# Kernel optimization log

Hardware: AMD Instinct MI355X
Metric: run time of the kernel (lower is better)

Reference implementation:

```python
import jax, jax.numpy as jnp
import numpy as np

K = 1024          # codebook size
D = 64            # embedding dim
CC = 0.25         # commitment cost


def setup_inputs() -> dict:
    key = jax.random.key(0)
    k1, k2 = jax.random.split(key)
    inputs = jax.random.normal(k1, (64, 64, 32, 32), dtype=jnp.float32)  # [B, C=D, H, W]
    # nn.Embedding weight init: uniform(-1/K, 1/K)
    embedding = jax.random.uniform(k2, (K, D), dtype=jnp.float32,
                                   minval=-1.0 / K, maxval=1.0 / K)
    return {"inputs": inputs, "embedding": embedding}


def reference(inputs, embedding):
    # NCHW -> NHWC
    x = jnp.transpose(inputs, (0, 2, 3, 1))            # [B, H, W, D]
    B, H, W, Dd = x.shape
    flat = x.reshape(-1, Dd)                           # [N, D]
    distances = (jnp.sum(flat * flat, axis=1, keepdims=True)
                 - 2.0 * flat @ embedding.T
                 + jnp.sum(embedding * embedding, axis=1)[None, :])
    encoding_indices = jnp.argmin(distances, axis=1)   # [N]
    encodings = encoding_indices.reshape(B, H, W)      # [B, H, W]
    quantized = embedding[encodings]                   # [B, H, W, D]

    e_latent_loss = jnp.mean((jax.lax.stop_gradient(quantized) - x) ** 2)
    q_latent_loss = jnp.mean((quantized - jax.lax.stop_gradient(x)) ** 2)
    loss = q_latent_loss + CC * e_latent_loss

    # straight-through estimator
    quantized_st = x + jax.lax.stop_gradient(quantized - x)
    out = jnp.transpose(quantized_st, (0, 3, 1, 2))    # NHWC -> NCHW
    nll = jnp.ones((1,), dtype=jnp.float32)
    return out, encodings, loss, nll
```

## Files before the change

kernel.cpp:

```cpp
#include <hip/hip_runtime.h>
#include <stdint.h>

constexpr int KCODES = 1024;
constexpr int DDIM   = 64;
constexpr int HW     = 1024;
constexpr int NPTS   = 65536;
constexpr int PPB    = 64;
constexpr int NBLK   = NPTS / PPB;

constexpr int OUT_IDX  = 4194304;
constexpr int OUT_LOSS = 4259840;
constexpr int OUT_NLL  = 4259841;

constexpr int WS_MAXC  = 0;
constexpr int WS_C     = 16;
constexpr int WS_E     = 2048;
constexpr int WS_PART  = 34816;

typedef __attribute__((ext_vector_type(8))) short short8v;
typedef __attribute__((ext_vector_type(4))) float float4v;

__device__ __forceinline__ uint16_t f2bf(float f) {
    uint32_t u = __float_as_uint(f);
    return (uint16_t)((u + 0x7fffu + ((u >> 16) & 1u)) >> 16);
}
__device__ __forceinline__ uint32_t pack2bf(float a, float b) {
    return (uint32_t)f2bf(a) | ((uint32_t)f2bf(b) << 16);
}

__device__ __forceinline__ float np_pairwise_sumsq64(const float* a) {
    float r[8];
    #pragma unroll
    for (int j = 0; j < 8; ++j) r[j] = __fmul_rn(a[j], a[j]);
    #pragma unroll
    for (int i = 8; i < 64; i += 8)
        #pragma unroll
        for (int j = 0; j < 8; ++j)
            r[j] = __fadd_rn(r[j], __fmul_rn(a[i + j], a[i + j]));
    return __fadd_rn(__fadd_rn(__fadd_rn(r[0], r[1]), __fadd_rn(r[2], r[3])),
                     __fadd_rn(__fadd_rn(r[4], r[5]), __fadd_rn(r[6], r[7])));
}

__global__ __launch_bounds__(64) void vq_init(const float* __restrict__ emb,
                                              float* __restrict__ ws) {
    const int k = blockIdx.x * 64 + threadIdx.x;
    float row[DDIM];
    const float4* src = (const float4*)(emb + (size_t)k * DDIM);
    #pragma unroll
    for (int j = 0; j < 16; ++j) ((float4*)row)[j] = src[j];
    float C = np_pairwise_sumsq64(row);
    ws[WS_C + k] = C;
    {
        const int c = k >> 4, col = k & 15;
        uint32_t* eb = (uint32_t*)ws + WS_E + c * 512;
        #pragma unroll
        for (int q = 0; q < 4; ++q) {
            uint32_t* d0 = eb + (q * 16 + col) * 4;
            uint32_t* d1 = eb + 256 + (q * 16 + col) * 4;
            #pragma unroll
            for (int j = 0; j < 4; ++j) {
                d0[j] = pack2bf(row[q * 8 + 2 * j],      row[q * 8 + 2 * j + 1]);
                d1[j] = pack2bf(row[32 + q * 8 + 2 * j], row[32 + q * 8 + 2 * j + 1]);
            }
        }
    }
    float m = C;
    #pragma unroll
    for (int off = 32; off > 0; off >>= 1) m = fmaxf(m, __shfl_down(m, off, 64));
    if (threadIdx.x == 0) ws[WS_MAXC + blockIdx.x] = m;
}

__global__ __launch_bounds__(256, 4) void vq_main(
        const float* __restrict__ inp, const float* __restrict__ emb,
        float* __restrict__ ws, float* __restrict__ out)
{
    __shared__ float    sAp[PPB][4];
    __shared__ float    sA[PPB];
    __shared__ float    sPart[4][PPB];
    __shared__ float    sThr[PPB];
    __shared__ unsigned long long sCandL[16][PPB];
    __shared__ int      sCntL[16][PPB];
    __shared__ int      sWin[PPB];
    __shared__ float    sred[4];

    const int tid  = threadIdx.x;
    const int lane = tid & 63;
    const int wave = tid >> 6;
    const int col  = lane & 15;
    const int quad = lane >> 4;
    const int base = blockIdx.x * PPB;
    const int b    = base >> 10;
    const int hw0  = base & 1023;

    {
        const int pp = tid >> 2;
        const int jj = (tid & 3) * 2;
        const float* xin = inp + (size_t)b * DDIM * HW + (hw0 + pp);
        float r0, r1;
        {
            float v0 = xin[(size_t)jj * HW];
            float v1 = xin[(size_t)(jj + 1) * HW];
            r0 = __fmul_rn(v0, v0);
            r1 = __fmul_rn(v1, v1);
        }
        #pragma unroll
        for (int i = 8; i < 64; i += 8) {
            float v0 = xin[(size_t)(i + jj) * HW];
            float v1 = xin[(size_t)(i + jj + 1) * HW];
            r0 = __fadd_rn(r0, __fmul_rn(v0, v0));
            r1 = __fadd_rn(r1, __fmul_rn(v1, v1));
        }
        sAp[pp][tid & 3] = __fadd_rn(r0, r1);
    }

    short8v a[4][2];
    #pragma unroll
    for (int g = 0; g < 4; ++g) {
        const float* xp = inp + (size_t)b * DDIM * HW + (hw0 + g * 16 + col);
        short8v t0, t1;
        #pragma unroll
        for (int j = 0; j < 8; ++j) {
            t0[j] = (short)f2bf(xp[(size_t)(quad * 8 + j) * HW]);
            t1[j] = (short)f2bf(xp[(size_t)(32 + quad * 8 + j) * HW]);
        }
        a[g][0] = t0; a[g][1] = t1;
    }

    const char* Eb = (const char*)((const uint32_t*)ws + WS_E);
    const char* Ew = Eb + (size_t)wave * 16 * 2048 + (size_t)lane * 16;
    const float* Cw = ws + WS_C;
    const int k0 = wave * 256;
    const float4v* Cq = (const float4v*)(ws + WS_C + k0);

    float gmax[4] = {-3.0e38f, -3.0e38f, -3.0e38f, -3.0e38f};
    {
        short8v pa0 = *(const short8v*)(Ew);
        short8v pa1 = *(const short8v*)(Ew + 1024);
        short8v pb0 = *(const short8v*)(Ew + 2048);
        short8v pb1 = *(const short8v*)(Ew + 3072);
        float4v ca4 = Cq[quad];
        float4v cb4 = Cq[4 + quad];
        #pragma unroll 1
        for (int c2 = 0; c2 < 16; c2 += 2) {
            short8v u0 = pa0, u1 = pa1; float4v uc4 = ca4;
            if (c2 + 2 < 16) {
                const char* er = Ew + (size_t)(c2 + 2) * 2048;
                pa0 = *(const short8v*)(er);
                pa1 = *(const short8v*)(er + 1024);
                ca4 = Cq[(c2 + 2) * 4 + quad];
            }
            {
                float4v ci = {uc4[0] * -0.5f, uc4[1] * -0.5f,
                              uc4[2] * -0.5f, uc4[3] * -0.5f};
                #pragma unroll
                for (int g = 0; g < 4; ++g) {
                    float4v acc = ci;
                    acc = __builtin_amdgcn_mfma_f32_16x16x32_bf16(u0, a[g][0], acc, 0, 0, 0);
                    acc = __builtin_amdgcn_mfma_f32_16x16x32_bf16(u1, a[g][1], acc, 0, 0, 0);
                    gmax[g] = fmaxf(gmax[g],
                                    fmaxf(fmaxf(acc[0], acc[1]), fmaxf(acc[2], acc[3])));
                }
            }
            short8v v0 = pb0, v1 = pb1; float4v vc4 = cb4;
            if (c2 + 3 < 16) {
                const char* er = Ew + (size_t)(c2 + 3) * 2048;
                pb0 = *(const short8v*)(er);
                pb1 = *(const short8v*)(er + 1024);
                cb4 = Cq[(c2 + 3) * 4 + quad];
            }
            {
                float4v ci = {vc4[0] * -0.5f, vc4[1] * -0.5f,
                              vc4[2] * -0.5f, vc4[3] * -0.5f};
                #pragma unroll
                for (int g = 0; g < 4; ++g) {
                    float4v acc = ci;
                    acc = __builtin_amdgcn_mfma_f32_16x16x32_bf16(v0, a[g][0], acc, 0, 0, 0);
                    acc = __builtin_amdgcn_mfma_f32_16x16x32_bf16(v1, a[g][1], acc, 0, 0, 0);
                    gmax[g] = fmaxf(gmax[g],
                                    fmaxf(fmaxf(acc[0], acc[1]), fmaxf(acc[2], acc[3])));
                }
            }
        }
    }
    #pragma unroll
    for (int g = 0; g < 4; ++g) {
        float m = gmax[g];
        m = fmaxf(m, __shfl_xor(m, 16, 64));
        m = fmaxf(m, __shfl_xor(m, 32, 64));
        if (quad == 0) sPart[wave][g * 16 + col] = m;
    }
    __syncthreads();

    if (tid < PPB) {
        float A = __fadd_rn(__fadd_rn(sAp[tid][0], sAp[tid][1]),
                            __fadd_rn(sAp[tid][2], sAp[tid][3]));
        sA[tid] = A;
        float gm = fmaxf(fmaxf(sPart[0][tid], sPart[1][tid]),
                         fmaxf(sPart[2][tid], sPart[3][tid]));
        float mc = ws[WS_MAXC];
        #pragma unroll
        for (int j = 1; j < 16; ++j) mc = fmaxf(mc, ws[WS_MAXC + j]);
        sThr[tid] = gm - (0.015625f * sqrtf(A) * sqrtf(mc) + 6e-5f);
    }
    __syncthreads();

    float thrg[4];
    #pragma unroll
    for (int g = 0; g < 4; ++g) thrg[g] = sThr[g * 16 + col];

    unsigned long long lst[4] = {0ull, 0ull, 0ull, 0ull};
    int cnt[4] = {0, 0, 0, 0};
    {
        short8v pa0 = *(const short8v*)(Ew);
        short8v pa1 = *(const short8v*)(Ew + 1024);
        short8v pb0 = *(const short8v*)(Ew + 2048);
        short8v pb1 = *(const short8v*)(Ew + 3072);
        float4v ca4 = Cq[quad];
        float4v cb4 = Cq[4 + quad];
        #pragma unroll 1
        for (int c2 = 0; c2 < 16; c2 += 2) {
            short8v u0 = pa0, u1 = pa1; float4v uc4 = ca4;
            if (c2 + 2 < 16) {
                const char* er = Ew + (size_t)(c2 + 2) * 2048;
                pa0 = *(const short8v*)(er);
                pa1 = *(const short8v*)(er + 1024);
                ca4 = Cq[(c2 + 2) * 4 + quad];
            }
            {
                float4v ci = {uc4[0] * -0.5f, uc4[1] * -0.5f,
                              uc4[2] * -0.5f, uc4[3] * -0.5f};
                const int kb = k0 + c2 * 16 + quad * 4;
                #pragma unroll
                for (int g = 0; g < 4; ++g) {
                    float4v acc = ci;
                    acc = __builtin_amdgcn_mfma_f32_16x16x32_bf16(u0, a[g][0], acc, 0, 0, 0);
                    acc = __builtin_amdgcn_mfma_f32_16x16x32_bf16(u1, a[g][1], acc, 0, 0, 0);
                    float m4 = fmaxf(fmaxf(acc[0], acc[1]), fmaxf(acc[2], acc[3]));
                    if (__any(m4 >= thrg[g])) {
                        #pragma unroll
                        for (int r = 0; r < 4; ++r) {
                            if (acc[r] >= thrg[g]) {
                                if (cnt[g] < 4)
                                    lst[g] |= (unsigned long long)(unsigned)(kb + r)
                                              << (cnt[g] << 4);
                                ++cnt[g];
                            }
                        }
                    }
                }
            }
            short8v v0 = pb0, v1 = pb1; float4v vc4 = cb4;
            if (c2 + 3 < 16) {
                const char* er = Ew + (size_t)(c2 + 3) * 2048;
                pb0 = *(const short8v*)(er);
                pb1 = *(const short8v*)(er + 1024);
                cb4 = Cq[(c2 + 3) * 4 + quad];
            }
            {
                float4v ci = {vc4[0] * -0.5f, vc4[1] * -0.5f,
                              vc4[2] * -0.5f, vc4[3] * -0.5f};
                const int kb = k0 + (c2 + 1) * 16 + quad * 4;
                #pragma unroll
                for (int g = 0; g < 4; ++g) {
                    float4v acc = ci;
                    acc = __builtin_amdgcn_mfma_f32_16x16x32_bf16(v0, a[g][0], acc, 0, 0, 0);
                    acc = __builtin_amdgcn_mfma_f32_16x16x32_bf16(v1, a[g][1], acc, 0, 0, 0);
                    float m4 = fmaxf(fmaxf(acc[0], acc[1]), fmaxf(acc[2], acc[3]));
                    if (__any(m4 >= thrg[g])) {
                        #pragma unroll
                        for (int r = 0; r < 4; ++r) {
                            if (acc[r] >= thrg[g]) {
                                if (cnt[g] < 4)
                                    lst[g] |= (unsigned long long)(unsigned)(kb + r)
                                              << (cnt[g] << 4);
                                ++cnt[g];
                            }
                        }
                    }
                }
            }
        }
    }
    {
        const int wq = wave * 4 + quad;
        #pragma unroll
        for (int g = 0; g < 4; ++g) {
            sCandL[wq][g * 16 + col] = lst[g];
            sCntL[wq][g * 16 + col]  = cnt[g];
        }
    }
    __syncthreads();

    if (tid < PPB) {
        const int p = tid, n = base + p;
        int tot = 0, cmax = 0;
        #pragma unroll
        for (int wq = 0; wq < 16; ++wq) {
            int c = sCntL[wq][p];
            tot += c;
            cmax = c > cmax ? c : cmax;
        }
        int win;
        if (tot == 1) {
            win = 0;
            #pragma unroll
            for (int wq = 0; wq < 16; ++wq)
                if (sCntL[wq][p]) win = (int)(sCandL[wq][p] & 0xffffu);
        } else {
            const float* xin = inp + (size_t)b * DDIM * HW + (hw0 + p);
            float x[DDIM];
            #pragma unroll
            for (int d = 0; d < DDIM; ++d) x[d] = xin[(size_t)d * HW];
            const float A = sA[p];
            float bd = 3.0e38f; win = KCODES - 1;
            if (cmax <= 4) {
                #pragma unroll 1
                for (int wq = 0; wq < 16; ++wq) {
                    int c = sCntL[wq][p];
                    unsigned long long L = sCandL[wq][p];
                    #pragma unroll 1
                    for (int i = 0; i < c; ++i) {
                        int k = (int)(L & 0xffffu);
                        L >>= 16;
                        float e[DDIM];
                        const float4* e4 = (const float4*)(emb + (size_t)k * DDIM);
                        #pragma unroll
                        for (int j = 0; j < 16; ++j) ((float4*)e)[j] = e4[j];
                        float g = 0.f;
                        #pragma unroll
                        for (int d = 0; d < DDIM; ++d) g = fmaf(x[d], e[d], g);
                        float dd = __fadd_rn(__fsub_rn(A, __fmul_rn(2.0f, g)), Cw[k]);
                        if (dd < bd || (dd == bd && k < win)) { bd = dd; win = k; }
                    }
                }
            } else {
                #pragma unroll 1
                for (int k = 0; k < KCODES; ++k) {
                    float e[DDIM];
                    const float4* e4 = (const float4*)(emb + (size_t)k * DDIM);
                    #pragma unroll
                    for (int j = 0; j < 16; ++j) ((float4*)e)[j] = e4[j];
                    float g = 0.f;
                    #pragma unroll
                    for (int d = 0; d < DDIM; ++d) g = fmaf(x[d], e[d], g);
                    float dd = __fadd_rn(__fsub_rn(A, __fmul_rn(2.0f, g)), Cw[k]);
                    if (dd < bd) { bd = dd; win = k; }
                }
            }
        }
        sWin[p] = win;
        out[OUT_IDX + n] = (float)win;
    }
    __syncthreads();

    {
        const int pl = tid & 63, qtr = tid >> 6;
        const int win = sWin[pl];
        const int ch0 = qtr * 16;
        float q[16];
        const float4* q4 = (const float4*)(emb + (size_t)win * DDIM + ch0);
        #pragma unroll
        for (int j = 0; j < 4; ++j) ((float4*)q)[j] = q4[j];
        const size_t off = (size_t)b * DDIM * HW + (size_t)ch0 * HW + (hw0 + pl);
        const float* xin2 = inp + off;
        float* orow = out + off;
        float lacc = 0.f;
        #pragma unroll
        for (int j = 0; j < 16; ++j) {
            float xv = xin2[(size_t)j * HW];
            float diff = __fsub_rn(q[j], xv);
            orow[(size_t)j * HW] = __fadd_rn(xv, diff);
            lacc = fmaf(diff, diff, lacc);
        }
        #pragma unroll
        for (int o2 = 32; o2 > 0; o2 >>= 1) lacc += __shfl_down(lacc, o2, 64);
        if (lane == 0) sred[wave] = lacc;
    }
    __syncthreads();
    if (tid == 0)
        ws[WS_PART + blockIdx.x] = sred[0] + sred[1] + sred[2] + sred[3];
}

__global__ __launch_bounds__(256) void vq_fin(const float* __restrict__ ws,
                                              float* __restrict__ out) {
    __shared__ float sred[4];
    const int tid = threadIdx.x;
    float s = 0.f;
    #pragma unroll
    for (int j = 0; j < 4; ++j) s += ws[WS_PART + j * 256 + tid];
    #pragma unroll
    for (int off = 32; off > 0; off >>= 1) s += __shfl_down(s, off, 64);
    if ((tid & 63) == 0) sred[tid >> 6] = s;
    __syncthreads();
    if (tid == 0) {
        float L = sred[0] + sred[1] + sred[2] + sred[3];
        out[OUT_LOSS] = L * (1.25f / 4194304.0f);
        out[OUT_NLL]  = 1.0f;
    }
}

extern "C" void kernel_launch(void* const* d_in, const int* in_sizes, int n_in,
                              void* d_out, int out_size, void* d_ws, size_t ws_size,
                              hipStream_t stream) {
    const float* inp = (const float*)d_in[0];
    const float* emb = (const float*)d_in[1];
    float* out = (float*)d_out;
    float* ws  = (float*)d_ws;

    vq_init<<<16, 64, 0, stream>>>(emb, ws);
    vq_main<<<NBLK, 256, 0, stream>>>(inp, emb, ws, out);
    vq_fin<<<1, 256, 0, stream>>>(ws, out);
}
```

Measured before the change: 114.5 us.

## Fuse max and candidate passes into single MFMA sweep with running-max top-4 slots

```diff
diff --git a/kernel.cpp b/kernel.cpp
--- a/kernel.cpp
+++ b/kernel.cpp
@@ -26,6 +26,36 @@
 }
 __device__ __forceinline__ uint32_t pack2bf(float a, float b) {
     return (uint32_t)f2bf(a) | ((uint32_t)f2bf(b) << 16);
+}
+
+__device__ __forceinline__ uint32_t bf_key(uint16_t b) {
+    return (uint32_t)b ^ (0x8000u + ((uint32_t)(b >> 15) * 0x7FFFu));
+}
+__device__ __forceinline__ float key_to_f32(uint32_t k16) {
+    uint32_t bb = (k16 & 0x8000u) ? (k16 ^ 0x8000u) : (~k16 & 0xFFFFu);
+    return __uint_as_float(bb << 16);
+}
+
+__device__ __forceinline__ void slot_insert(uint32_t& s0, uint32_t& s1,
+                                            uint32_t& s2, uint32_t& s3,
+                                            uint32_t& ovfg, float s, int idx,
+                                            float mnew, float marE) {
+    uint32_t key  = bf_key(f2bf(s));
+    uint32_t slot = (key << 16) | (uint32_t)idx;
+    uint32_t m01 = s0 < s1 ? s0 : s1;
+    uint32_t m23 = s2 < s3 ? s2 : s3;
+    uint32_t mm  = m01 < m23 ? m01 : m23;
+    float mf = key_to_f32(mm >> 16);
+    bool safe = (mm < 0x10000u) || (mf < mnew - marE);
+    ovfg |= safe ? 0u : 1u;
+    bool p0 = (s0 == mm);
+    bool p1 = !p0 && (s1 == mm);
+    bool p2 = !p0 && !p1 && (s2 == mm);
+    bool p3 = !(p0 || p1 || p2);
+    s0 = p0 ? slot : s0;
+    s1 = p1 ? slot : s1;
+    s2 = p2 ? slot : s2;
+    s3 = p3 ? slot : s3;
 }
 
 __device__ __forceinline__ float np_pairwise_sumsq64(const float* a) {
@@ -76,10 +106,13 @@
 {
     __shared__ float    sAp[PPB][4];
     __shared__ float    sA[PPB];
+    __shared__ float    sMar[PPB];
+    __shared__ float    sMarE[PPB];
+    __shared__ float    sEps[PPB];
     __shared__ float    sPart[4][PPB];
     __shared__ float    sThr[PPB];
-    __shared__ unsigned long long sCandL[16][PPB];
-    __shared__ int      sCntL[16][PPB];
+    __shared__ uint32_t sSlot[16][PPB][4];
+    __shared__ uint8_t  sOvf[16][PPB];
     __shared__ int      sWin[PPB];
     __shared__ float    sred[4];
 
@@ -125,6 +158,30 @@
         }
         a[g][0] = t0; a[g][1] = t1;
     }
+    __syncthreads();
+
+    if (tid < PPB) {
+        float A = __fadd_rn(__fadd_rn(sAp[tid][0], sAp[tid][1]),
+                            __fadd_rn(sAp[tid][2], sAp[tid][3]));
+        sA[tid] = A;
+        float mc = ws[WS_MAXC];
+        #pragma unroll
+        for (int j = 1; j < 16; ++j) mc = fmaxf(mc, ws[WS_MAXC + j]);
+        float sq = sqrtf(A) * sqrtf(mc);
+        float M  = 0.015625f * sq + 6e-5f;
+        float E  = 0.0078125f * sq + 0.001953125f * mc;
+        sMar[tid]  = M;
+        sMarE[tid] = M + E;
+        sEps[tid]  = E;
+    }
+    __syncthreads();
+
+    float marg[4], marE[4];
+    #pragma unroll
+    for (int g = 0; g < 4; ++g) {
+        marg[g] = sMar[g * 16 + col];
+        marE[g] = sMarE[g * 16 + col];
+    }
 
     const char* Eb = (const char*)((const uint32_t*)ws + WS_E);
     const char* Ew = Eb + (size_t)wave * 16 * 2048 + (size_t)lane * 16;
@@ -132,7 +189,9 @@
     const int k0 = wave * 256;
     const float4v* Cq = (const float4v*)(ws + WS_C + k0);
 
-    float gmax[4] = {-3.0e38f, -3.0e38f, -3.0e38f, -3.0e38f};
+    float    m_run[4] = {-3.0e38f, -3.0e38f, -3.0e38f, -3.0e38f};
+    uint32_t sl[4][4] = {{0,0,0,0},{0,0,0,0},{0,0,0,0},{0,0,0,0}};
+    uint32_t ovf[4]   = {0,0,0,0};
     {
         short8v pa0 = *(const short8v*)(Ew);
         short8v pa1 = *(const short8v*)(Ew + 1024);
@@ -152,83 +211,6 @@
             {
                 float4v ci = {uc4[0] * -0.5f, uc4[1] * -0.5f,
                               uc4[2] * -0.5f, uc4[3] * -0.5f};
-                #pragma unroll
-                for (int g = 0; g < 4; ++g) {
-                    float4v acc = ci;
-                    acc = __builtin_amdgcn_mfma_f32_16x16x32_bf16(u0, a[g][0], acc, 0, 0, 0);
-                    acc = __builtin_amdgcn_mfma_f32_16x16x32_bf16(u1, a[g][1], acc, 0, 0, 0);
-                    gmax[g] = fmaxf(gmax[g],
-                                    fmaxf(fmaxf(acc[0], acc[1]), fmaxf(acc[2], acc[3])));
-                }
-            }
-            short8v v0 = pb0, v1 = pb1; float4v vc4 = cb4;
-            if (c2 + 3 < 16) {
-                const char* er = Ew + (size_t)(c2 + 3) * 2048;
-                pb0 = *(const short8v*)(er);
-                pb1 = *(const short8v*)(er + 1024);
-                cb4 = Cq[(c2 + 3) * 4 + quad];
-            }
-            {
-                float4v ci = {vc4[0] * -0.5f, vc4[1] * -0.5f,
-                              vc4[2] * -0.5f, vc4[3] * -0.5f};
-                #pragma unroll
-                for (int g = 0; g < 4; ++g) {
-                    float4v acc = ci;
-                    acc = __builtin_amdgcn_mfma_f32_16x16x32_bf16(v0, a[g][0], acc, 0, 0, 0);
-                    acc = __builtin_amdgcn_mfma_f32_16x16x32_bf16(v1, a[g][1], acc, 0, 0, 0);
-                    gmax[g] = fmaxf(gmax[g],
-                                    fmaxf(fmaxf(acc[0], acc[1]), fmaxf(acc[2], acc[3])));
-                }
-            }
-        }
-    }
-    #pragma unroll
-    for (int g = 0; g < 4; ++g) {
-        float m = gmax[g];
-        m = fmaxf(m, __shfl_xor(m, 16, 64));
-        m = fmaxf(m, __shfl_xor(m, 32, 64));
-        if (quad == 0) sPart[wave][g * 16 + col] = m;
-    }
-    __syncthreads();
-
-    if (tid < PPB) {
-        float A = __fadd_rn(__fadd_rn(sAp[tid][0], sAp[tid][1]),
-                            __fadd_rn(sAp[tid][2], sAp[tid][3]));
-        sA[tid] = A;
-        float gm = fmaxf(fmaxf(sPart[0][tid], sPart[1][tid]),
-                         fmaxf(sPart[2][tid], sPart[3][tid]));
-        float mc = ws[WS_MAXC];
-        #pragma unroll
-        for (int j = 1; j < 16; ++j) mc = fmaxf(mc, ws[WS_MAXC + j]);
-        sThr[tid] = gm - (0.015625f * sqrtf(A) * sqrtf(mc) + 6e-5f);
-    }
-    __syncthreads();
-
-    float thrg[4];
-    #pragma unroll
-    for (int g = 0; g < 4; ++g) thrg[g] = sThr[g * 16 + col];
-
-    unsigned long long lst[4] = {0ull, 0ull, 0ull, 0ull};
-    int cnt[4] = {0, 0, 0, 0};
-    {
-        short8v pa0 = *(const short8v*)(Ew);
-        short8v pa1 = *(const short8v*)(Ew + 1024);
-        short8v pb0 = *(const short8v*)(Ew + 2048);
-        short8v pb1 = *(const short8v*)(Ew + 3072);
-        float4v ca4 = Cq[quad];
-        float4v cb4 = Cq[4 + quad];
-        #pragma unroll 1
-        for (int c2 = 0; c2 < 16; c2 += 2) {
-            short8v u0 = pa0, u1 = pa1; float4v uc4 = ca4;
-            if (c2 + 2 < 16) {
-                const char* er = Ew + (size_t)(c2 + 2) * 2048;
-                pa0 = *(const short8v*)(er);
-                pa1 = *(const short8v*)(er + 1024);
-                ca4 = Cq[(c2 + 2) * 4 + quad];
-            }
-            {
-                float4v ci = {uc4[0] * -0.5f, uc4[1] * -0.5f,
-                              uc4[2] * -0.5f, uc4[3] * -0.5f};
                 const int kb = k0 + c2 * 16 + quad * 4;
                 #pragma unroll
                 for (int g = 0; g < 4; ++g) {
@@ -236,16 +218,14 @@
                     acc = __builtin_amdgcn_mfma_f32_16x16x32_bf16(u0, a[g][0], acc, 0, 0, 0);
                     acc = __builtin_amdgcn_mfma_f32_16x16x32_bf16(u1, a[g][1], acc, 0, 0, 0);
                     float m4 = fmaxf(fmaxf(acc[0], acc[1]), fmaxf(acc[2], acc[3]));
-                    if (__any(m4 >= thrg[g])) {
+                    float mnew = fmaxf(m_run[g], m4);
+                    m_run[g] = mnew;
+                    if (__any(m4 >= mnew - marg[g])) {
                         #pragma unroll
-                        for (int r = 0; r < 4; ++r) {
-                            if (acc[r] >= thrg[g]) {
-                                if (cnt[g] < 4)
-                                    lst[g] |= (unsigned long long)(unsigned)(kb + r)
-                                              << (cnt[g] << 4);
-                                ++cnt[g];
-                            }
-                        }
+                        for (int r = 0; r < 4; ++r)
+                            if (acc[r] >= mnew - marg[g])
+                                slot_insert(sl[g][0], sl[g][1], sl[g][2], sl[g][3],
+                                            ovf[g], acc[r], kb + r, mnew, marE[g]);
                     }
                 }
             }
@@ -266,46 +246,90 @@
                     acc = __builtin_amdgcn_mfma_f32_16x16x32_bf16(v0, a[g][0], acc, 0, 0, 0);
                     acc = __builtin_amdgcn_mfma_f32_16x16x32_bf16(v1, a[g][1], acc, 0, 0, 0);
                     float m4 = fmaxf(fmaxf(acc[0], acc[1]), fmaxf(acc[2], acc[3]));
-                    if (__any(m4 >= thrg[g])) {
+                    float mnew = fmaxf(m_run[g], m4);
+                    m_run[g] = mnew;
+                    if (__any(m4 >= mnew - marg[g])) {
                         #pragma unroll
-                        for (int r = 0; r < 4; ++r) {
-                            if (acc[r] >= thrg[g]) {
-                                if (cnt[g] < 4)
-                                    lst[g] |= (unsigned long long)(unsigned)(kb + r)
-                                              << (cnt[g] << 4);
-                                ++cnt[g];
-                            }
-                        }
+                        for (int r = 0; r < 4; ++r)
+                            if (acc[r] >= mnew - marg[g])
+                                slot_insert(sl[g][0], sl[g][1], sl[g][2], sl[g][3],
+                                            ovf[g], acc[r], kb + r, mnew, marE[g]);
                     }
                 }
             }
         }
     }
+    #pragma unroll
+    for (int g = 0; g < 4; ++g) {
+        float m = m_run[g];
+        m = fmaxf(m, __shfl_xor(m, 16, 64));
+        m = fmaxf(m, __shfl_xor(m, 32, 64));
+        if (quad == 0) sPart[wave][g * 16 + col] = m;
+    }
     {
         const int wq = wave * 4 + quad;
         #pragma unroll
         for (int g = 0; g < 4; ++g) {
-            sCandL[wq][g * 16 + col] = lst[g];
-            sCntL[wq][g * 16 + col]  = cnt[g];
-        }
+            uint32_t* d = &sSlot[wq][g * 16 + col][0];
+            d[0] = sl[g][0]; d[1] = sl[g][1]; d[2] = sl[g][2]; d[3] = sl[g][3];
+            sOvf[wq][g * 16 + col] = (uint8_t)ovf[g];
+        }
+    }
+    __syncthreads();
+
+    if (tid < PPB) {
+        float gm = fmaxf(fmaxf(sPart[0][tid], sPart[1][tid]),
+                         fmaxf(sPart[2][tid], sPart[3][tid]));
+        sThr[tid] = gm - sMar[tid];
     }
     __syncthreads();
 
     if (tid < PPB) {
         const int p = tid, n = base + p;
-        int tot = 0, cmax = 0;
-        #pragma unroll
+        const float thrE = sThr[p] - sEps[p];
+        bool ovfAny = false;
+        #pragma unroll
+        for (int wq = 0; wq < 16; ++wq) ovfAny |= (sOvf[wq][p] != 0);
+        int tot = 0, first = 0;
+        #pragma unroll 1
         for (int wq = 0; wq < 16; ++wq) {
-            int c = sCntL[wq][p];
-            tot += c;
-            cmax = c > cmax ? c : cmax;
+            #pragma unroll
+            for (int j = 0; j < 4; ++j) {
+                uint32_t s = sSlot[wq][p][j];
+                float f = key_to_f32(s >> 16);
+                if (f >= thrE) { ++tot; if (tot == 1) first = (int)(s & 0xFFFFu); }
+            }
         }
         int win;
-        if (tot == 1) {
-            win = 0;
+        if (!ovfAny && tot == 1) {
+            win = first;
+        } else if (!ovfAny && tot >= 2) {
+            const float* xin = inp + (size_t)b * DDIM * HW + (hw0 + p);
+            float x[DDIM];
             #pragma unroll
-            for (int wq = 0; wq < 16; ++wq)
-                if (sCntL[wq][p]) win = (int)(sCandL[wq][p] & 0xffffu);
+            for (int d = 0; d < DDIM; ++d) x[d] = xin[(size_t)d * HW];
+            const float A = sA[p];
+            float bd = 3.0e38f; win = KCODES - 1;
+            #pragma unroll 1
+            for (int wq = 0; wq < 16; ++wq) {
+                #pragma unroll
+                for (int j = 0; j < 4; ++j) {
+                    uint32_t s = sSlot[wq][p][j];
+                    float f = key_to_f32(s >> 16);
+                    if (f >= thrE) {
+                        int k = (int)(s & 0xFFFFu);
+                        float e[DDIM];
+                        const float4* e4 = (const float4*)(emb + (size_t)k * DDIM);
+                        #pragma unroll
+                        for (int jj = 0; jj < 16; ++jj) ((float4*)e)[jj] = e4[jj];
+                        float g = 0.f;
+                        #pragma unroll
+                        for (int d = 0; d < DDIM; ++d) g = fmaf(x[d], e[d], g);
+                        float dd = __fadd_rn(__fsub_rn(A, __fmul_rn(2.0f, g)), Cw[k]);
+                        if (dd < bd || (dd == bd && k < win)) { bd = dd; win = k; }
+                    }
+                }
+            }
         } else {
             const float* xin = inp + (size_t)b * DDIM * HW + (hw0 + p);
             float x[DDIM];
@@ -313,39 +337,17 @@
             for (int d = 0; d < DDIM; ++d) x[d] = xin[(size_t)d * HW];
             const float A = sA[p];
             float bd = 3.0e38f; win = KCODES - 1;
-            if (cmax <= 4) {
-                #pragma unroll 1
-                for (int wq = 0; wq < 16; ++wq) {
-                    int c = sCntL[wq][p];
-                    unsigned long long L = sCandL[wq][p];
-                    #pragma unroll 1
-                    for (int i = 0; i < c; ++i) {
-                        int k = (int)(L & 0xffffu);
-                        L >>= 16;
-                        float e[DDIM];
-                        const float4* e4 = (const float4*)(emb + (size_t)k * DDIM);
-                        #pragma unroll
-                        for (int j = 0; j < 16; ++j) ((float4*)e)[j] = e4[j];
-                        float g = 0.f;
-                        #pragma unroll
-                        for (int d = 0; d < DDIM; ++d) g = fmaf(x[d], e[d], g);
-                        float dd = __fadd_rn(__fsub_rn(A, __fmul_rn(2.0f, g)), Cw[k]);
-                        if (dd < bd || (dd == bd && k < win)) { bd = dd; win = k; }
-                    }
-                }
-            } else {
-                #pragma unroll 1
-                for (int k = 0; k < KCODES; ++k) {
-                    float e[DDIM];
-                    const float4* e4 = (const float4*)(emb + (size_t)k * DDIM);
-                    #pragma unroll
-                    for (int j = 0; j < 16; ++j) ((float4*)e)[j] = e4[j];
-                    float g = 0.f;
-                    #pragma unroll
-                    for (int d = 0; d < DDIM; ++d) g = fmaf(x[d], e[d], g);
-                    float dd = __fadd_rn(__fsub_rn(A, __fmul_rn(2.0f, g)), Cw[k]);
-                    if (dd < bd) { bd = dd; win = k; }
-                }
+            #pragma unroll 1
+            for (int k = 0; k < KCODES; ++k) {
+                float e[DDIM];
+                const float4* e4 = (const float4*)(emb + (size_t)k * DDIM);
+                #pragma unroll
+                for (int j = 0; j < 16; ++j) ((float4*)e)[j] = e4[j];
+                float g = 0.f;
+                #pragma unroll
+                for (int d = 0; d < DDIM; ++d) g = fmaf(x[d], e[d], g);
+                float dd = __fadd_rn(__fsub_rn(A, __fmul_rn(2.0f, g)), Cw[k]);
+                if (dd < bd) { bd = dd; win = k; }
             }
         }
         sWin[p] = win;
```

New measurement: 436.6 us. 281% more time.

## Double points per block to reuse codebook fragments across more MFMAs

Applied to the files above, without the earlier changes.

```diff
diff --git a/kernel.cpp b/kernel.cpp
--- a/kernel.cpp
+++ b/kernel.cpp
@@ -5,7 +5,7 @@
 constexpr int DDIM   = 64;
 constexpr int HW     = 1024;
 constexpr int NPTS   = 65536;
-constexpr int PPB    = 64;
+constexpr int PPB    = 128;
 constexpr int NBLK   = NPTS / PPB;
 
 constexpr int OUT_IDX  = 4194304;
@@ -70,18 +70,18 @@
     if (threadIdx.x == 0) ws[WS_MAXC + blockIdx.x] = m;
 }
 
-__global__ __launch_bounds__(256, 4) void vq_main(
+__global__ __launch_bounds__(256, 2) void vq_main(
         const float* __restrict__ inp, const float* __restrict__ emb,
         float* __restrict__ ws, float* __restrict__ out)
 {
-    __shared__ float    sAp[PPB][4];
+    __shared__ float    sAp[PPB][2];
     __shared__ float    sA[PPB];
     __shared__ float    sPart[4][PPB];
     __shared__ float    sThr[PPB];
     __shared__ unsigned long long sCandL[16][PPB];
     __shared__ int      sCntL[16][PPB];
     __shared__ int      sWin[PPB];
-    __shared__ float    sred[4];
+    __shared__ float    sred2[2][4];
 
     const int tid  = threadIdx.x;
     const int lane = tid & 63;
@@ -93,29 +93,36 @@
     const int hw0  = base & 1023;
 
     {
-        const int pp = tid >> 2;
-        const int jj = (tid & 3) * 2;
+        const int pp = tid & 127;
+        const int hh = tid >> 7;
+        const int j0 = hh * 4;
         const float* xin = inp + (size_t)b * DDIM * HW + (hw0 + pp);
-        float r0, r1;
+        float r0, r1, r2, r3;
         {
-            float v0 = xin[(size_t)jj * HW];
-            float v1 = xin[(size_t)(jj + 1) * HW];
-            r0 = __fmul_rn(v0, v0);
-            r1 = __fmul_rn(v1, v1);
+            float v0 = xin[(size_t)(j0 + 0) * HW];
+            float v1 = xin[(size_t)(j0 + 1) * HW];
+            float v2 = xin[(size_t)(j0 + 2) * HW];
+            float v3 = xin[(size_t)(j0 + 3) * HW];
+            r0 = __fmul_rn(v0, v0); r1 = __fmul_rn(v1, v1);
+            r2 = __fmul_rn(v2, v2); r3 = __fmul_rn(v3, v3);
         }
         #pragma unroll
         for (int i = 8; i < 64; i += 8) {
-            float v0 = xin[(size_t)(i + jj) * HW];
-            float v1 = xin[(size_t)(i + jj + 1) * HW];
+            float v0 = xin[(size_t)(i + j0 + 0) * HW];
+            float v1 = xin[(size_t)(i + j0 + 1) * HW];
+            float v2 = xin[(size_t)(i + j0 + 2) * HW];
+            float v3 = xin[(size_t)(i + j0 + 3) * HW];
             r0 = __fadd_rn(r0, __fmul_rn(v0, v0));
             r1 = __fadd_rn(r1, __fmul_rn(v1, v1));
-        }
-        sAp[pp][tid & 3] = __fadd_rn(r0, r1);
-    }
-
-    short8v a[4][2];
-    #pragma unroll
-    for (int g = 0; g < 4; ++g) {
+            r2 = __fadd_rn(r2, __fmul_rn(v2, v2));
+            r3 = __fadd_rn(r3, __fmul_rn(v3, v3));
+        }
+        sAp[pp][hh] = __fadd_rn(__fadd_rn(r0, r1), __fadd_rn(r2, r3));
+    }
+
+    short8v a[8][2];
+    #pragma unroll
+    for (int g = 0; g < 8; ++g) {
         const float* xp = inp + (size_t)b * DDIM * HW + (hw0 + g * 16 + col);
         short8v t0, t1;
         #pragma unroll
@@ -132,7 +139,8 @@
     const int k0 = wave * 256;
     const float4v* Cq = (const float4v*)(ws + WS_C + k0);
 
-    float gmax[4] = {-3.0e38f, -3.0e38f, -3.0e38f, -3.0e38f};
+    float gmax[8] = {-3.0e38f, -3.0e38f, -3.0e38f, -3.0e38f,
+                     -3.0e38f, -3.0e38f, -3.0e38f, -3.0e38f};
     {
         short8v pa0 = *(const short8v*)(Ew);
         short8v pa1 = *(const short8v*)(Ew + 1024);
@@ -153,7 +161,7 @@
                 float4v ci = {uc4[0] * -0.5f, uc4[1] * -0.5f,
                               uc4[2] * -0.5f, uc4[3] * -0.5f};
                 #pragma unroll
-                for (int g = 0; g < 4; ++g) {
+                for (int g = 0; g < 8; ++g) {
                     float4v acc = ci;
                     acc = __builtin_amdgcn_mfma_f32_16x16x32_bf16(u0, a[g][0], acc, 0, 0, 0);
                     acc = __builtin_amdgcn_mfma_f32_16x16x32_bf16(u1, a[g][1], acc, 0, 0, 0);
@@ -172,7 +180,7 @@
                 float4v ci = {vc4[0] * -0.5f, vc4[1] * -0.5f,
                               vc4[2] * -0.5f, vc4[3] * -0.5f};
                 #pragma unroll
-                for (int g = 0; g < 4; ++g) {
+                for (int g = 0; g < 8; ++g) {
                     float4v acc = ci;
                     acc = __builtin_amdgcn_mfma_f32_16x16x32_bf16(v0, a[g][0], acc, 0, 0, 0);
                     acc = __builtin_amdgcn_mfma_f32_16x16x32_bf16(v1, a[g][1], acc, 0, 0, 0);
@@ -183,7 +191,7 @@
         }
     }
     #pragma unroll
-    for (int g = 0; g < 4; ++g) {
+    for (int g = 0; g < 8; ++g) {
         float m = gmax[g];
         m = fmaxf(m, __shfl_xor(m, 16, 64));
         m = fmaxf(m, __shfl_xor(m, 32, 64));
@@ -192,8 +200,7 @@
     __syncthreads();
 
     if (tid < PPB) {
-        float A = __fadd_rn(__fadd_rn(sAp[tid][0], sAp[tid][1]),
-                            __fadd_rn(sAp[tid][2], sAp[tid][3]));
+        float A = __fadd_rn(sAp[tid][0], sAp[tid][1]);
         sA[tid] = A;
         float gm = fmaxf(fmaxf(sPart[0][tid], sPart[1][tid]),
                          fmaxf(sPart[2][tid], sPart[3][tid]));
@@ -204,12 +211,12 @@
     }
     __syncthreads();
 
-    float thrg[4];
-    #pragma unroll
-    for (int g = 0; g < 4; ++g) thrg[g] = sThr[g * 16 + col];
-
-    unsigned long long lst[4] = {0ull, 0ull, 0ull, 0ull};
-    int cnt[4] = {0, 0, 0, 0};
+    float thrg[8];
+    #pragma unroll
+    for (int g = 0; g < 8; ++g) thrg[g] = sThr[g * 16 + col];
+
+    unsigned long long lst[8] = {0,0,0,0,0,0,0,0};
+    int cnt[8] = {0,0,0,0,0,0,0,0};
     {
         short8v pa0 = *(const short8v*)(Ew);
         short8v pa1 = *(const short8v*)(Ew + 1024);
@@ -231,7 +238,7 @@
                               uc4[2] * -0.5f, uc4[3] * -0.5f};
                 const int kb = k0 + c2 * 16 + quad * 4;
                 #pragma unroll
-                for (int g = 0; g < 4; ++g) {
+                for (int g = 0; g < 8; ++g) {
                     float4v acc = ci;
                     acc = __builtin_amdgcn_mfma_f32_16x16x32_bf16(u0, a[g][0], acc, 0, 0, 0);
                     acc = __builtin_amdgcn_mfma_f32_16x16x32_bf16(u1, a[g][1], acc, 0, 0, 0);
@@ -261,7 +268,7 @@
                               vc4[2] * -0.5f, vc4[3] * -0.5f};
                 const int kb = k0 + (c2 + 1) * 16 + quad * 4;
                 #pragma unroll
-                for (int g = 0; g < 4; ++g) {
+                for (int g = 0; g < 8; ++g) {
                     float4v acc = ci;
                     acc = __builtin_amdgcn_mfma_f32_16x16x32_bf16(v0, a[g][0], acc, 0, 0, 0);
                     acc = __builtin_amdgcn_mfma_f32_16x16x32_bf16(v1, a[g][1], acc, 0, 0, 0);
@@ -284,7 +291,7 @@
     {
         const int wq = wave * 4 + quad;
         #pragma unroll
-        for (int g = 0; g < 4; ++g) {
+        for (int g = 0; g < 8; ++g) {
             sCandL[wq][g * 16 + col] = lst[g];
             sCntL[wq][g * 16 + col]  = cnt[g];
         }
@@ -353,15 +360,17 @@
     }
     __syncthreads();
 
-    {
+    #pragma unroll 1
+    for (int h = 0; h < 2; ++h) {
         const int pl = tid & 63, qtr = tid >> 6;
-        const int win = sWin[pl];
+        const int win = sWin[h * 64 + pl];
         const int ch0 = qtr * 16;
         float q[16];
         const float4* q4 = (const float4*)(emb + (size_t)win * DDIM + ch0);
         #pragma unroll
         for (int j = 0; j < 4; ++j) ((float4*)q)[j] = q4[j];
-        const size_t off = (size_t)b * DDIM * HW + (size_t)ch0 * HW + (hw0 + pl);
+        const size_t off = (size_t)b * DDIM * HW + (size_t)ch0 * HW
+                           + (hw0 + h * 64 + pl);
         const float* xin2 = inp + off;
         float* orow = out + off;
         float lacc = 0.f;
@@ -374,11 +383,15 @@
         }
         #pragma unroll
         for (int o2 = 32; o2 > 0; o2 >>= 1) lacc += __shfl_down(lacc, o2, 64);
-        if (lane == 0) sred[wave] = lacc;
-    }
-    __syncthreads();
-    if (tid == 0)
-        ws[WS_PART + blockIdx.x] = sred[0] + sred[1] + sred[2] + sred[3];
+        if ((tid & 63) == 0) sred2[h][qtr] = lacc;
+    }
+    __syncthreads();
+    if (tid == 0) {
+        ws[WS_PART + 2 * blockIdx.x + 0] =
+            sred2[0][0] + sred2[0][1] + sred2[0][2] + sred2[0][3];
+        ws[WS_PART + 2 * blockIdx.x + 1] =
+            sred2[1][0] + sred2[1][1] + sred2[1][2] + sred2[1][3];
+    }
 }
 
 __global__ __launch_bounds__(256) void vq_fin(const float* __restrict__ ws,
```

After: 117.9 us. +3.0%, slower.
